# Performance work log

Hardware: AMD Instinct MI355X
Metric: run time of the kernel (lower is better)

## Reference

```python
import jax, jax.numpy as jnp
import numpy as np

N, C, T, V = 128, 256, 48, 25
CR = C // 16
SEG = 3
BN_EPS = 1e-5


def setup_inputs() -> dict:
    key = jax.random.key(0)
    ks = jax.random.split(key, 8)
    s = lambda k, shape: jax.random.normal(k, shape, dtype=jnp.float32) * 0.05
    return {
        "x": jax.random.normal(ks[0], (N, C, T, V), dtype=jnp.float32),
        "w_sq": s(ks[1], (CR, C)),   # me_squeeze 1x1 conv weight [out,in]
        "b_sq": s(ks[2], (CR,)),
        "gamma": jnp.ones((CR,), jnp.float32),   # BN weight
        "beta": jnp.zeros((CR,), jnp.float32),   # BN bias
        "rmean": jnp.zeros((CR,), jnp.float32),  # BN running mean
        "rvar": jnp.ones((CR,), jnp.float32),    # BN running var
        "w_c1": s(ks[3], (CR, CR)),  # me_conv1 1x1 conv weight
        "b_c1": s(ks[4], (CR,)),
        "w_ex": s(ks[5], (C, CR)),   # me_expand 1x1 conv weight
        "b_ex": s(ks[6], (C,)),
    }


def reference(x, w_sq, b_sq, gamma, beta, rmean, rvar, w_c1, b_c1, w_ex, b_ex):
    n, c, t, v = x.shape
    nb = (n * t) // SEG
    cr = w_sq.shape[0]
    # 1x1 squeeze conv + BatchNorm (eval mode, running stats) -> [n, cr, t, v]
    y = jnp.einsum('nctv,rc->nrtv', x, w_sq) + b_sq[None, :, None, None]
    scale = gamma / jnp.sqrt(rvar + BN_EPS)
    y = y * scale[None, :, None, None] + (beta - rmean * scale)[None, :, None, None]
    # 1x1 conv on squeezed features (shifted branch)
    y1 = jnp.einsum('nrtv,sr->nstv', y, w_c1) + b_c1[None, :, None, None]
    # regroup consecutive frames into segments of SEG along time: (n*t) -> (nb, SEG)
    yseg = y.transpose(0, 2, 1, 3).reshape(nb, SEG, cr, v)
    y1seg = y1.transpose(0, 2, 1, 3).reshape(nb, SEG, cr, v)
    # temporal difference: conv(frame k+1) - frame k, zero-pad last frame of each segment
    diff = y1seg[:, 1:] - yseg[:, :SEG - 1]                    # [nb, SEG-1, cr, v]
    diff = jnp.pad(diff, ((0, 0), (0, 1), (0, 0), (0, 0)))     # [nb, SEG, cr, v]
    x_me = diff.reshape(n, t, cr, v).transpose(0, 2, 1, 3)     # [n, cr, t, v]
    # adaptive avg pool over joints (v -> 1), expand conv, sigmoid gate
    m = jnp.mean(x_me, axis=-1, keepdims=True)                 # [n, cr, t, 1]
    gate = jax.nn.sigmoid(jnp.einsum('nrtu,cr->nctu', m, w_ex) + b_ex[None, :, None, None])
    return x * gate
```

## Files before the change

kernel.cpp:

```cpp
#include <hip/hip_runtime.h>

typedef float v4f __attribute__((ext_vector_type(4)));

__global__ __launch_bounds__(512, 4) void k_fused11(
    const float* __restrict__ x,
    const float* __restrict__ wsq, const float* __restrict__ bsq,
    const float* __restrict__ gamma, const float* __restrict__ beta,
    const float* __restrict__ rmean, const float* __restrict__ rvar,
    const float* __restrict__ wc1, const float* __restrict__ bc1,
    const float* __restrict__ wex, const float* __restrict__ bex,
    float* __restrict__ out)
{
    __shared__ v4f   wb[8][2][152];
    __shared__ float xb[12 * 260];
    __shared__ float part[384];
    __shared__ float ybn[192], y1[192], mv[192];

    float* wsqL = (float*)wb;
    float* gs   = (float*)wb + 4352;

    const int tid = threadIdx.x;
    const int w   = tid >> 6;
    const int ln  = tid & 63;
    const unsigned bid = blockIdx.x;
    const unsigned o = (bid & 7u) * 64u + (bid >> 3);
    const unsigned n = o >> 2;
    const unsigned q = o & 3u;

    const v4f* x4 = (const v4f*)x + (size_t)n * 76800u + q * 75u;
    v4f*       o4 = (v4f*)out     + (size_t)n * 76800u + q * 75u;

    const int crBase = w * 32;

    v4f sA[3], sB[3];
    auto issueW = [&](int rnd, v4f* st) {
        int cr = crBase + rnd * 2;
        #pragma unroll
        for (int qq = 0; qq < 3; ++qq) {
            int s = qq * 64 + ln;
            if (s < 150) {
                int c = cr + (s >= 75 ? 1 : 0);
                int k = (s >= 75) ? s - 75 : s;
                st[qq] = x4[c * 300 + k];
            }
        }
    };
    auto writeW = [&](int rnd, const v4f* st) {
        v4f* dst = wb[w][rnd & 1];
        #pragma unroll
        for (int qq = 0; qq < 3; ++qq) {
            int s = qq * 64 + ln;
            if (s < 150) dst[s] = st[qq];
        }
    };
    auto reduceW = [&](int rnd) {
        if (ln < 24) {
            int co = ln / 12, t = ln - co * 12;
            const float* bp = (const float*)wb[w][rnd & 1] + co * 300 + t * 25;
            float s = 0.f;
            #pragma unroll
            for (int v = 0; v < 25; ++v) s += bp[v];
            xb[t * 260 + crBase + rnd * 2 + co] = s;
        }
    };

    issueW(0, sA);
    issueW(1, sB);
    #pragma unroll
    for (int r = 0; r < 16; r += 2) {
        writeW(r, sA);
        if (r + 2 < 16) issueW(r + 2, sA);
        reduceW(r);
        writeW(r + 1, sB);
        if (r + 3 < 16) issueW(r + 3, sB);
        reduceW(r + 1);
    }
    __syncthreads();

    #pragma unroll
    for (int it = 0; it < 8; ++it) {
        int j = it * 512 + tid;
        wsqL[(j & 255) * 17 + (j >> 8)] = wsq[j];
    }
    __syncthreads();

    if (tid < 384) {
        int t = tid >> 5, rh = tid & 31, r = rh >> 1, hh = rh & 1;
        float acc = 0.f;
        #pragma unroll 8
        for (int i = 0; i < 128; ++i)
            acc += xb[t * 260 + hh * 128 + i] * wsqL[(hh * 128 + i) * 17 + r];
        part[tid] = acc;
    }
    __syncthreads();
    if (tid < 192) {
        int t = tid >> 4, r = tid & 15;
        float acc = part[t * 32 + r * 2] + part[t * 32 + r * 2 + 1];
        float sc = gamma[r] * rsqrtf(rvar[r] + 1e-5f);
        ybn[tid] = acc * (0.04f * sc) + (bsq[r] * sc + beta[r] - rmean[r] * sc);
    }
    __syncthreads();
    if (tid < 192) {
        int t = tid >> 4, s = tid & 15;
        float a = bc1[s];
        #pragma unroll
        for (int r = 0; r < 16; ++r) a += ybn[t * 16 + r] * wc1[s * 16 + r];
        y1[tid] = a;
    }
    __syncthreads();
    if (tid < 192) {
        int t = tid >> 4;
        mv[tid] = ((t % 3) < 2) ? (y1[tid + 16] - ybn[tid]) : 0.f;
    }
    __syncthreads();
    {
        int c = tid & 255, half = tid >> 8;
        float wexr[16];
        #pragma unroll
        for (int r = 0; r < 16; ++r) wexr[r] = wex[c * 16 + r];
        float be = bex[c];
        #pragma unroll
        for (int t = half * 6; t < half * 6 + 6; ++t) {
            float a = be;
            #pragma unroll
            for (int r = 0; r < 16; ++r) a += mv[t * 16 + r] * wexr[r];
            gs[c * 12 + t] = 1.f / (1.f + expf(-a));
        }
    }
    __syncthreads();

    #pragma unroll 4
    for (int it = 0; it < 38; ++it) {
        int j = it * 512 + tid;
        if (j < 19200) {
            unsigned c = ((unsigned)j * 55926u) >> 22;
            int k = j - (int)c * 75;
            v4f v = x4[c * 300 + k];
            int m0  = k * 4;
            int t0  = (m0 * 41) >> 10;
            int t3  = ((m0 + 3) * 41) >> 10;
            int rem = m0 - t0 * 25;
            float g0 = gs[c * 12 + t0];
            float g3 = gs[c * 12 + t3];
            v4f ov;
            ov.x = v.x * g0;
            ov.y = v.y * ((rem + 1 < 25) ? g0 : g3);
            ov.z = v.z * ((rem + 2 < 25) ? g0 : g3);
            ov.w = v.w * ((rem + 3 < 25) ? g0 : g3);
            __builtin_nontemporal_store(ov, &o4[c * 300 + k]);
        }
    }
}

extern "C" void kernel_launch(void* const* d_in, const int* in_sizes, int n_in,
                              void* d_out, int out_size, void* d_ws, size_t ws_size,
                              hipStream_t stream) {
    const float* x     = (const float*)d_in[0];
    const float* wsq   = (const float*)d_in[1];
    const float* bsq   = (const float*)d_in[2];
    const float* gamma = (const float*)d_in[3];
    const float* beta  = (const float*)d_in[4];
    const float* rmean = (const float*)d_in[5];
    const float* rvar  = (const float*)d_in[6];
    const float* wc1   = (const float*)d_in[7];
    const float* bc1   = (const float*)d_in[8];
    const float* wex   = (const float*)d_in[9];
    const float* bex   = (const float*)d_in[10];

    k_fused11<<<512, 512, 0, stream>>>(x, wsq, bsq, gamma, beta,
                                       rmean, rvar, wc1, bc1, wex, bex,
                                       (float*)d_out);
}
```

Measured before the change: 79.49 us.

## Stream x tiles into LDS via global_load_lds with triple-buffered block-wide pipeline

The first pass over x now uses direct global-to-LDS DMA loads (global_load_lds) into a three-stage ring buffer shared by the whole block. Before, each wave staged data through registers and copied it into per-wave LDS buffers. Each stage covers 16 channels, and block barriers with explicit vmcnt waits handle the synchronisation. The aim is to drop the register round-trip and keep more loads in flight. The squeeze conv also reads wsq straight from global instead of transposing it into LDS first. In exchange, the change adds a block-wide barrier per channel group and relies on hand-tuned vmcnt counts, which are fragile.

```diff
diff --git a/kernel.cpp b/kernel.cpp
--- a/kernel.cpp
+++ b/kernel.cpp
@@ -2,7 +2,11 @@
 
 typedef float v4f __attribute__((ext_vector_type(4)));
 
-__global__ __launch_bounds__(512, 4) void k_fused11(
+#define GLD(g, l) __builtin_amdgcn_global_load_lds( \
+    (const __attribute__((address_space(1))) void*)(g), \
+    (__attribute__((address_space(3))) void*)(l), 16, 0, 0)
+
+__global__ __launch_bounds__(512, 4) void k_dma3(
     const float* __restrict__ x,
     const float* __restrict__ wsq, const float* __restrict__ bsq,
     const float* __restrict__ gamma, const float* __restrict__ beta,
@@ -11,17 +15,14 @@
     const float* __restrict__ wex, const float* __restrict__ bex,
     float* __restrict__ out)
 {
-    __shared__ v4f   wb[8][2][152];
+    __shared__ v4f   buf[3][1216];
     __shared__ float xb[12 * 260];
     __shared__ float part[384];
     __shared__ float ybn[192], y1[192], mv[192];
-
-    float* wsqL = (float*)wb;
-    float* gs   = (float*)wb + 4352;
+    float* gs = (float*)buf;
 
     const int tid = threadIdx.x;
     const int w   = tid >> 6;
-    const int ln  = tid & 63;
     const unsigned bid = blockIdx.x;
     const unsigned o = (bid & 7u) * 64u + (bid >> 3);
     const unsigned n = o >> 2;
@@ -30,66 +31,59 @@
     const v4f* x4 = (const v4f*)x + (size_t)n * 76800u + q * 75u;
     v4f*       o4 = (v4f*)out     + (size_t)n * 76800u + q * 75u;
 
-    const int crBase = w * 32;
-
-    v4f sA[3], sB[3];
-    auto issueW = [&](int rnd, v4f* st) {
-        int cr = crBase + rnd * 2;
+    auto issue = [&](int cg) {
+        v4f* dst = buf[cg % 3];
         #pragma unroll
-        for (int qq = 0; qq < 3; ++qq) {
-            int s = qq * 64 + ln;
-            if (s < 150) {
-                int c = cr + (s >= 75 ? 1 : 0);
-                int k = (s >= 75) ? s - 75 : s;
-                st[qq] = x4[c * 300 + k];
+        for (int it = 0; it < 3; ++it) {
+            int s = it * 512 + tid;
+            if (it < 2 || w < 3) {
+                int sc = (s < 1200) ? s : 1199;
+                int c = sc / 75, k = sc - c * 75;
+                GLD(x4 + (cg * 16 + c) * 300 + k, dst + s);
             }
         }
     };
-    auto writeW = [&](int rnd, const v4f* st) {
-        v4f* dst = wb[w][rnd & 1];
-        #pragma unroll
-        for (int qq = 0; qq < 3; ++qq) {
-            int s = qq * 64 + ln;
-            if (s < 150) dst[s] = st[qq];
-        }
-    };
-    auto reduceW = [&](int rnd) {
-        if (ln < 24) {
-            int co = ln / 12, t = ln - co * 12;
-            const float* bp = (const float*)wb[w][rnd & 1] + co * 300 + t * 25;
+    auto reduceC = [&](int cg) {
+        if (tid < 192) {
+            int t = tid >> 4, cl = tid & 15;
+            const float* bp = (const float*)buf[cg % 3] + cl * 300 + t * 25;
             float s = 0.f;
             #pragma unroll
             for (int v = 0; v < 25; ++v) s += bp[v];
-            xb[t * 260 + crBase + rnd * 2 + co] = s;
+            xb[t * 260 + cg * 16 + cl] = s;
         }
     };
 
-    issueW(0, sA);
-    issueW(1, sB);
-    #pragma unroll
-    for (int r = 0; r < 16; r += 2) {
-        writeW(r, sA);
-        if (r + 2 < 16) issueW(r + 2, sA);
-        reduceW(r);
-        writeW(r + 1, sB);
-        if (r + 3 < 16) issueW(r + 3, sB);
-        reduceW(r + 1);
-    }
-    __syncthreads();
+    issue(0);
+    issue(1);
+    if (w < 3) asm volatile("s_waitcnt vmcnt(3)" ::: "memory");
+    else       asm volatile("s_waitcnt vmcnt(2)" ::: "memory");
+    __builtin_amdgcn_s_barrier();
+    __builtin_amdgcn_sched_barrier(0);
 
     #pragma unroll
-    for (int it = 0; it < 8; ++it) {
-        int j = it * 512 + tid;
-        wsqL[(j & 255) * 17 + (j >> 8)] = wsq[j];
+    for (int i = 0; i < 16; ++i) {
+        if (i + 2 < 16) issue(i + 2);
+        reduceC(i);
+        if (i < 15) {
+            if (i + 2 < 16) {
+                if (w < 3) asm volatile("s_waitcnt vmcnt(3)" ::: "memory");
+                else       asm volatile("s_waitcnt vmcnt(2)" ::: "memory");
+            } else {
+                asm volatile("s_waitcnt vmcnt(0)" ::: "memory");
+            }
+            __builtin_amdgcn_s_barrier();
+            __builtin_amdgcn_sched_barrier(0);
+        }
     }
     __syncthreads();
 
     if (tid < 384) {
         int t = tid >> 5, rh = tid & 31, r = rh >> 1, hh = rh & 1;
+        const float* wrow = wsq + r * 256 + hh * 128;
         float acc = 0.f;
         #pragma unroll 8
-        for (int i = 0; i < 128; ++i)
-            acc += xb[t * 260 + hh * 128 + i] * wsqL[(hh * 128 + i) * 17 + r];
+        for (int i = 0; i < 128; ++i) acc += xb[t * 260 + hh * 128 + i] * wrow[i];
         part[tid] = acc;
     }
     __syncthreads();
@@ -167,7 +161,7 @@
     const float* wex   = (const float*)d_in[9];
     const float* bex   = (const float*)d_in[10];
 
-    k_fused11<<<512, 512, 0, stream>>>(x, wsq, bsq, gamma, beta,
-                                       rmean, rvar, wc1, bc1, wex, bex,
-                                       (float*)d_out);
+    k_dma3<<<512, 512, 0, stream>>>(x, wsq, bsq, gamma, beta,
+                                    rmean, rvar, wc1, bc1, wex, bex,
+                                    (float*)d_out);
 }
```

After: 86.70 us. +9.1%, slower.
